# Optimization experiments

Hardware: AMD Instinct MI355X
Metric: run time of the kernel (lower is better)

Reference implementation:

```python
import jax, jax.numpy as jnp
import numpy as np

D_MODEL, D_HEAD, N_HEAD, PERIOD = 1024, 64, 16, 30
B, T1, T2 = 2, 2048, 2048


def setup_inputs() -> dict:
    key = jax.random.key(0)
    ks = jax.random.split(key, 7)
    s_in = 1.0 / np.sqrt(D_MODEL)
    s_out = 1.0 / np.sqrt(N_HEAD * D_HEAD)
    return {
        "x": jax.random.normal(ks[0], (B, T1, D_MODEL), dtype=jnp.float32),
        "context": jax.random.normal(ks[1], (B, T2, D_MODEL), dtype=jnp.float32),
        "Wq": jax.random.uniform(ks[2], (N_HEAD * D_HEAD, D_MODEL), jnp.float32, -s_in, s_in),
        "Wk": jax.random.uniform(ks[3], (N_HEAD * D_HEAD, D_MODEL), jnp.float32, -s_in, s_in),
        "Wv": jax.random.uniform(ks[4], (N_HEAD * D_HEAD, D_MODEL), jnp.float32, -s_in, s_in),
        "Wo": jax.random.uniform(ks[5], (D_MODEL, N_HEAD * D_HEAD), jnp.float32, -s_out, s_out),
        "bo": jax.random.uniform(ks[6], (D_MODEL,), jnp.float32, -s_out, s_out),
    }


def reference(x, context, Wq, Wk, Wv, Wo, bo):
    Bx, T1x, _ = x.shape
    T2x = context.shape[1]
    scale = 1.0 / np.sqrt(D_HEAD).astype(np.float32)
    # projections (torch Linear: y = x @ W^T)
    q = (x @ Wq.T).reshape(Bx, T1x, N_HEAD, D_HEAD)
    k = (context @ Wk.T).reshape(Bx, T2x, N_HEAD, D_HEAD)
    v = (context @ Wv.T).reshape(Bx, T2x, N_HEAD, D_HEAD)
    # attention scores [B, H, T1, T2]
    scores = jnp.einsum('bihd,bjhd->bhij', q, k) * scale
    # ALiBi-style periodic distance bias
    dist = jnp.abs(jnp.arange(T1x)[:, None] - jnp.arange(T2x)[None, :])  # [T1,T2]
    bias = -(dist // PERIOD).astype(jnp.float32)                          # [T1,T2]
    head_scale = jnp.power(2.0, -jnp.arange(1, N_HEAD + 1, dtype=jnp.float32))
    biased = scores + bias[None, None, :, :] * head_scale[None, :, None, None]
    attn = jax.nn.softmax(biased, axis=-1)
    out = jnp.einsum('bhij,bjhd->bihd', attn, v).reshape(Bx, T1x, N_HEAD * D_HEAD)
    # output projection; dropout is identity in eval mode
    return out @ Wo.T + bo
```

## Files before the change

### kernel.cpp

```cpp
#include <hip/hip_runtime.h>
#include <hip/hip_fp16.h>

typedef _Float16 f16;
typedef __attribute__((ext_vector_type(8))) _Float16 f16x8;
typedef __attribute__((ext_vector_type(4))) _Float16 f16x4;
typedef __attribute__((ext_vector_type(2))) __fp16 fp16x2;
typedef __attribute__((ext_vector_type(4))) float f32x4;
typedef __attribute__((ext_vector_type(16))) float f32x16;

#define DM 1024
#define NH 16
#define DH 64
#define TT 2048
#define LOG2E 1.4426950408889634f
#define QSCALE 0.18033688f

#define SB0 __builtin_amdgcn_sched_barrier(0)
#define LGKM0 asm volatile("s_waitcnt lgkmcnt(0)" ::: "memory")

__global__ __launch_bounds__(256) void cvt_all(const float* __restrict__ x, const float* __restrict__ cx,
                                               const float* __restrict__ wq, const float* __restrict__ wk,
                                               const float* __restrict__ wv, const float* __restrict__ wo,
                                               f16* __restrict__ xb, f16* __restrict__ cb,
                                               f16* __restrict__ wqb, f16* __restrict__ wkb,
                                               f16* __restrict__ wvb, f16* __restrict__ wob,
                                               f16* __restrict__ FBf) {
  int idx = blockIdx.x * 256 + threadIdx.x;
  int stride = gridDim.x * 256;
  for (int i = idx; i < 3670016; i += stride) {
    if (i >= 3145728) {
      int c = i - 3145728;
      int half = c & 1, lane = (c >> 1) & 63, kvt = (c >> 7) & 63, qt = c >> 13;
      int qi = qt * 32 + (lane & 31);
      int jb = kvt * 32 + 16 * half + 8 * (lane >> 5);
      f16x8 v;
#pragma unroll
      for (int e = 0; e < 8; e++) {
        int d = qi - (jb + e); d = (d < 0) ? -d : d;
        v[e] = (f16)(d / 30);
      }
      reinterpret_cast<f16x8*>(FBf)[c] = v;
      continue;
    }
    const float* src; f16* dst; int off; float s = 1.0f;
    if (i < 2097152) {
      if (i < 1048576) { src = x; dst = xb; off = i; }
      else { src = cx; dst = cb; off = i - 1048576; }
    } else {
      int j = i - 2097152;
      int wsel = j >> 18;
      off = j & 262143;
      if (wsel == 0) { src = wq; dst = wqb; s = QSCALE; }
      else if (wsel == 1) { src = wk; dst = wkb; }
      else if (wsel == 2) { src = wv; dst = wvb; }
      else { src = wo; dst = wob; }
    }
    float4 v = reinterpret_cast<const float4*>(src)[off];
    f16x4 o = { (f16)(v.x * s), (f16)(v.y * s), (f16)(v.z * s), (f16)(v.w * s) };
    reinterpret_cast<f16x4*>(dst)[off] = o;
  }
}

__device__ __forceinline__ void gemm_mainloop(const f16* __restrict__ A, const f16* __restrict__ W,
                                              int bm, int bn, f16 (*As)[4096], f16 (*Bs)[4096],
                                              f32x4 (&acc)[4][4]) {
  int t = threadIdx.x;
  int w = t >> 6;
  int lane = t & 63, lr = lane & 15, g = lane >> 4;
  int wr = w >> 1, wc = w & 1;
  int scol = ((t & 3) ^ ((t >> 3) & 3)) * 8;
  const f16* a0 = A + (size_t)(bm + (t >> 2)) * DM + scol;
  const f16* a1 = a0 + (size_t)64 * DM;
  const f16* b0 = W + (size_t)(bn + (t >> 2)) * DM + scol;
  const f16* b1 = b0 + (size_t)64 * DM;
  int szg = ((lr >> 1) & 3) << 4;

  f16x8 rA0, rA1, rB0, rB1;
  auto LOADR = [&](int kt) {
    rA0 = *reinterpret_cast<const f16x8*>(a0 + kt);
    rA1 = *reinterpret_cast<const f16x8*>(a1 + kt);
    rB0 = *reinterpret_cast<const f16x8*>(b0 + kt);
    rB1 = *reinterpret_cast<const f16x8*>(b1 + kt);
  };
  auto WRITE = [&](int bufi) {
    char* Ab = (char*)As[bufi];
    char* Bb = (char*)Bs[bufi];
    *reinterpret_cast<f16x8*>(Ab + t * 16) = rA0;
    *reinterpret_cast<f16x8*>(Ab + 4096 + t * 16) = rA1;
    *reinterpret_cast<f16x8*>(Bb + t * 16) = rB0;
    *reinterpret_cast<f16x8*>(Bb + 4096 + t * 16) = rB1;
  };
  auto CMPG = [&](int bufi) {
    const char* Ab = (const char*)As[bufi];
    const char* Bb = (const char*)Bs[bufi];
    f16x8 af[4], bf[4];
#pragma unroll
    for (int mi = 0; mi < 4; mi++) {
      int row = wr * 64 + mi * 16 + lr;
      af[mi] = *reinterpret_cast<const f16x8*>(Ab + row * 64 + ((g << 4) ^ szg));
    }
#pragma unroll
    for (int ni = 0; ni < 4; ni++) {
      int row = wc * 64 + ni * 16 + lr;
      bf[ni] = *reinterpret_cast<const f16x8*>(Bb + row * 64 + ((g << 4) ^ szg));
    }
    __builtin_amdgcn_s_setprio(1);
#pragma unroll
    for (int mi = 0; mi < 4; mi++)
#pragma unroll
      for (int ni = 0; ni < 4; ni++)
        acc[mi][ni] = __builtin_amdgcn_mfma_f32_16x16x32_f16(af[mi], bf[ni], acc[mi][ni], 0, 0, 0);
    __builtin_amdgcn_s_setprio(0);
  };

  LOADR(0);
  WRITE(0);
  LOADR(32);
  LGKM0;
  __builtin_amdgcn_s_barrier();
  SB0;

#pragma unroll 1
  for (int tp = 0; tp < 16; tp++) {
    int s0 = 2 * tp;
    CMPG(0);
    WRITE(1);
    if (s0 + 2 < 32) LOADR((s0 + 2) * 32);
    LGKM0;
    __builtin_amdgcn_s_barrier();
    SB0;
    CMPG(1);
    if (s0 + 2 < 32) {
      WRITE(0);
      if (s0 + 3 < 32) LOADR((s0 + 3) * 32);
      LGKM0;
      __builtin_amdgcn_s_barrier();
      SB0;
    }
  }
}

__global__ __launch_bounds__(256) void qkv_gemm(const f16* __restrict__ xb, const f16* __restrict__ cb,
                                                const f16* __restrict__ wq, const f16* __restrict__ wk,
                                                const f16* __restrict__ wv,
                                                f16* __restrict__ Qo, f16* __restrict__ Ko,
                                                f16* __restrict__ Vt) {
  __shared__ f16 As[2][4096];
  __shared__ f16 Bs[2][4096];
  int o = blockIdx.x;
  int lin = (o & 7) * 96 + (o >> 3);
  int gid = lin >> 8;
  int bid = lin & 255;
  int bm = (bid >> 3) * 128, bn = (bid & 7) * 128;
  const f16* A = (gid == 0) ? xb : cb;
  const f16* W = (gid == 0) ? wq : ((gid == 1) ? wk : wv);
  f32x4 acc[4][4] = {};
  gemm_mainloop(A, W, bm, bn, As, Bs, acc);

  int t = threadIdx.x, w = t >> 6, lane = t & 63, lr = lane & 15, g = lane >> 4;
  int wr = w >> 1, wc = w & 1;
  if (gid < 2) {
    f16* out = (gid == 0) ? Qo : Ko;
#pragma unroll
    for (int mi = 0; mi < 4; mi++) {
      int m0 = bm + wr * 64 + mi * 16 + 4 * g;
      int b = m0 >> 11, i0 = m0 & 2047;
#pragma unroll
      for (int ni = 0; ni < 4; ni++) {
        int n = bn + wc * 64 + ni * 16 + lr;
        int h = n >> 6, d = n & 63;
        size_t base = (((size_t)(b * NH + h)) * TT + i0) * DH + d;
#pragma unroll
        for (int r = 0; r < 4; r++)
          out[base + (size_t)r * DH] = (f16)acc[mi][ni][r];
      }
    }
  } else {
#pragma unroll
    for (int mi = 0; mi < 4; mi++) {
      int m0 = bm + wr * 64 + mi * 16 + 4 * g;
      int b = m0 >> 11, j0 = m0 & 2047;
#pragma unroll
      for (int ni = 0; ni < 4; ni++) {
        int n = bn + wc * 64 + ni * 16 + lr;
        int h = n >> 6, d = n & 63;
        f16x4 pk = { (f16)acc[mi][ni][0], (f16)acc[mi][ni][1],
                     (f16)acc[mi][ni][2], (f16)acc[mi][ni][3] };
        *reinterpret_cast<f16x4*>(&Vt[(((size_t)(b * NH + h)) * DH + d) * TT + j0]) = pk;
      }
    }
  }
}

__global__ __launch_bounds__(256) void out_gemm(const f16* __restrict__ Ob, const f16* __restrict__ wo,
                                                const float* __restrict__ bo, float* __restrict__ Y) {
  __shared__ f16 As[2][4096];
  __shared__ f16 Bs[2][4096];
  int o = blockIdx.x;
  int bid = (o & 7) * 32 + (o >> 3);
  int bm = (bid >> 3) * 128, bn = (bid & 7) * 128;
  f32x4 acc[4][4] = {};
  gemm_mainloop(Ob, wo, bm, bn, As, Bs, acc);
  int t = threadIdx.x, w = t >> 6, lane = t & 63, lr = lane & 15, g = lane >> 4;
  int wr = w >> 1, wc = w & 1;
#pragma unroll
  for (int mi = 0; mi < 4; mi++) {
    int m0 = bm + wr * 64 + mi * 16 + 4 * g;
#pragma unroll
    for (int ni = 0; ni < 4; ni++) {
      int n = bn + wc * 64 + ni * 16 + lr;
      float bias = bo[n];
#pragma unroll
      for (int r = 0; r < 4; r++)
        Y[(size_t)(m0 + r) * DM + n] = acc[mi][ni][r] + bias;
    }
  }
}

struct FB4 { f16x8 a, b, c, d; };

__global__ __launch_bounds__(256, 2) void attn_kernel(const f16* __restrict__ Q, const f16* __restrict__ K,
                                                      const f16* __restrict__ V, const f16* __restrict__ FBf,
                                                      f16* __restrict__ O) {
  __shared__ f16 KV[2][8192];
  int o = blockIdx.x;
  int xcd = o & 7, idx = o >> 3;
  int bh = 4 * xcd + (idx >> 4), qblk = idx & 15;
  int h = bh & 15, b = bh >> 4;
  int tt = threadIdx.x, w = tt >> 6, lane = tt & 63;
  int col = lane & 31, hi = lane >> 5;
  int qi = qblk * 128 + w * 32 + col;

  const f16* qp = Q + ((size_t)bh * TT + qi) * DH + hi * 8;
  f16x8 qf[4];
#pragma unroll
  for (int s = 0; s < 4; s++) qf[s] = *reinterpret_cast<const f16x8*>(qp + 16 * s);

  const float nc2 = -exp2f(-(float)(h + 1)) * LOG2E;
  int qtp = qblk * 4 + w;
  const f16x8* fbp = reinterpret_cast<const f16x8*>(FBf) + ((size_t)qtp << 13) + (lane << 1);

  f32x4 rsv = { 0.f, 0.f, 0.f, 0.f };
  f32x16 oacc0 = {}, oacc1 = {};

  int rho0 = tt >> 3, G = tt & 7;
  int f0 = (rho0 & 7) ^ (3 * ((rho0 >> 4) & 1));
  int J0 = (rho0 & 19) | ((rho0 & 4) << 1) | ((rho0 & 8) >> 1);
  const f16* kp0 = K + ((size_t)bh * TT + J0) * DH + (G ^ f0) * 8;
  const f16* kp1 = K + ((size_t)bh * TT + 32 + J0) * DH + (G ^ f0) * 8;
  const f16* vp0 = V + ((size_t)bh * DH + rho0) * TT + (G ^ f0) * 8;
  const f16* vp1 = V + ((size_t)bh * DH + 32 + rho0) * TT + (G ^ f0) * 8;

  f16x8 r0, r1, r2, r3;
  auto LOADR = [&](int kv0) {
    r0 = *reinterpret_cast<const f16x8*>(kp0 + (size_t)kv0 * DH);
    r1 = *reinterpret_cast<const f16x8*>(kp1 + (size_t)kv0 * DH);
    r2 = *reinterpret_cast<const f16x8*>(vp0 + kv0);
    r3 = *reinterpret_cast<const f16x8*>(vp1 + kv0);
  };
  auto WRITE = [&](int bufi) {
    char* base = (char*)KV[bufi];
    *reinterpret_cast<f16x8*>(base + tt * 16) = r0;
    *reinterpret_cast<f16x8*>(base + 4096 + tt * 16) = r1;
    *reinterpret_cast<f16x8*>(base + 8192 + tt * 16) = r2;
    *reinterpret_cast<f16x8*>(base + 12288 + tt * 16) = r3;
  };

  int fcol = (col & 7) ^ (3 * ((col >> 4) & 1));
  int kb0 = col * 128;
  int ksw[4];
#pragma unroll
  for (int s = 0; s < 4; s++) ksw[s] = ((2 * s + hi) ^ fcol) << 4;

  auto FBLOAD = [&](int t) {
    FB4 f;
    f.a = fbp[256 * t];
    f.b = fbp[256 * t + 1];
    f.c = fbp[256 * t + 128];
    f.d = fbp[256 * t + 129];
    return f;
  };

  auto CMP = [&](int bufi, const FB4& fb) {
    const char* Kb = (const char*)KV[bufi];
    f32x16 S0 = {}, S1 = {};
    __builtin_amdgcn_s_setprio(1);
#pragma unroll
    for (int s = 0; s < 4; s++) {
      f16x8 ka0 = *reinterpret_cast<const f16x8*>(Kb + kb0 + ksw[s]);
      f16x8 ka1 = *reinterpret_cast<const f16x8*>(Kb + 4096 + kb0 + ksw[s]);
      S0 = __builtin_amdgcn_mfma_f32_32x32x16_f16(ka0, qf[s], S0, 0, 0, 0);
      S1 = __builtin_amdgcn_mfma_f32_32x32x16_f16(ka1, qf[s], S1, 0, 0, 0);
    }
    __builtin_amdgcn_s_setprio(0);
    float p0[16], p1[16];
#pragma unroll
    for (int r = 0; r < 16; r++) {
      float fb0 = (float)((r < 8) ? fb.a[r] : fb.b[r - 8]);
      float fb1 = (float)((r < 8) ? fb.c[r] : fb.d[r - 8]);
      p0[r] = __builtin_amdgcn_exp2f(fmaf(fb0, nc2, S0[r]));
      p1[r] = __builtin_amdgcn_exp2f(fmaf(fb1, nc2, S1[r]));
    }
#pragma unroll
    for (int r = 0; r < 4; r++) {
      f32x4 pa = { p0[4 * r], p0[4 * r + 1], p0[4 * r + 2], p0[4 * r + 3] };
      f32x4 pc = { p1[4 * r], p1[4 * r + 1], p1[4 * r + 2], p1[4 * r + 3] };
      rsv += pa + pc;
    }
    f16x8 pb[4];
#pragma unroll
    for (int s2 = 0; s2 < 2; s2++) {
      union { f16x8 v; fp16x2 hh[4]; } u0, u1;
#pragma unroll
      for (int q2 = 0; q2 < 4; q2++) {
        u0.hh[q2] = __builtin_amdgcn_cvt_pkrtz(p0[8 * s2 + 2 * q2], p0[8 * s2 + 2 * q2 + 1]);
        u1.hh[q2] = __builtin_amdgcn_cvt_pkrtz(p1[8 * s2 + 2 * q2], p1[8 * s2 + 2 * q2 + 1]);
      }
      pb[s2] = u0.v; pb[2 + s2] = u1.v;
    }
    __builtin_amdgcn_s_setprio(1);
#pragma unroll
    for (int s2 = 0; s2 < 4; s2++) {
      f16x8 va0 = *reinterpret_cast<const f16x8*>(Kb + 8192 + kb0 + ksw[s2]);
      f16x8 va1 = *reinterpret_cast<const f16x8*>(Kb + 12288 + kb0 + ksw[s2]);
      oacc0 = __builtin_amdgcn_mfma_f32_32x32x16_f16(va0, pb[s2], oacc0, 0, 0, 0);
      oacc1 = __builtin_amdgcn_mfma_f32_32x32x16_f16(va1, pb[s2], oacc1, 0, 0, 0);
    }
    __builtin_amdgcn_s_setprio(0);
  };

  LOADR(0);
  WRITE(0);
  LOADR(64);
  FB4 fA = FBLOAD(0);
  FB4 fB = FBLOAD(1);
  LGKM0;
  __builtin_amdgcn_s_barrier();
  SB0;

#pragma unroll 1
  for (int tp = 0; tp < 16; tp++) {
    int t0 = 2 * tp;
    CMP(0, fA);
    WRITE(1);
    if (t0 + 2 < 32) { LOADR((t0 + 2) << 6); fA = FBLOAD(t0 + 2); }
    LGKM0;
    __builtin_amdgcn_s_barrier();
    SB0;
    CMP(1, fB);
    if (t0 + 2 < 32) {
      WRITE(0);
      if (t0 + 3 < 32) { LOADR((t0 + 3) << 6); fB = FBLOAD(t0 + 3); }
      LGKM0;
      __builtin_amdgcn_s_barrier();
      SB0;
    }
  }

  float lsum = (rsv[0] + rsv[1]) + (rsv[2] + rsv[3]);
  lsum += __shfl_xor(lsum, 32, 64);
  float inv = __builtin_amdgcn_rcpf(lsum);

  size_t ob = ((size_t)b * TT + qi) * DM + h * DH + 4 * hi;
  const f32x16* oa[2] = { &oacc0, &oacc1 };
#pragma unroll
  for (int db = 0; db < 2; db++)
#pragma unroll
    for (int a = 0; a < 4; a++) {
      f16x4 o4 = { (f16)((*oa[db])[4 * a] * inv),     (f16)((*oa[db])[4 * a + 1] * inv),
                   (f16)((*oa[db])[4 * a + 2] * inv), (f16)((*oa[db])[4 * a + 3] * inv) };
      *reinterpret_cast<f16x4*>(&O[ob + 32 * db + 8 * a]) = o4;
    }
}

extern "C" void kernel_launch(void* const* d_in, const int* in_sizes, int n_in,
                              void* d_out, int out_size, void* d_ws, size_t ws_size,
                              hipStream_t stream) {
  const float* x  = (const float*)d_in[0];
  const float* cx = (const float*)d_in[1];
  const float* Wq = (const float*)d_in[2];
  const float* Wk = (const float*)d_in[3];
  const float* Wv = (const float*)d_in[4];
  const float* Wo = (const float*)d_in[5];
  const float* bo = (const float*)d_in[6];
  float* Y = (float*)d_out;

  const size_t NTOK = (size_t)2 * TT;
  f16* p = (f16*)d_ws;
  f16* xb  = p; p += NTOK * DM;
  f16* cb  = p; p += NTOK * DM;
  f16* wqb = p; p += (size_t)DM * DM;
  f16* wkb = p; p += (size_t)DM * DM;
  f16* wvb = p; p += (size_t)DM * DM;
  f16* wob = p; p += (size_t)DM * DM;
  f16* Qb  = p; p += NTOK * DM;
  f16* Kb  = p; p += NTOK * DM;
  f16* Vtb = p; p += NTOK * DM;
  f16* Ob  = p; p += NTOK * DM;
  f16* FBt = p;

  cvt_all<<<2048, 256, 0, stream>>>(x, cx, Wq, Wk, Wv, Wo, xb, cb, wqb, wkb, wvb, wob, FBt);
  qkv_gemm<<<768, 256, 0, stream>>>(xb, cb, wqb, wkb, wvb, Qb, Kb, Vtb);
  attn_kernel<<<512, 256, 0, stream>>>(Qb, Kb, Vtb, FBt, Ob);
  out_gemm<<<256, 256, 0, stream>>>(Ob, wob, bo, Y);
}
```

Before: 124.6 us.

## Split attention KV range in two and merge partial results in output GEMM

The attention grid doubles so each block handles half of the key/value sequence. Each block writes an unnormalized f16 partial output plus its row sum, and the occupancy hint rises from 2 to 4 blocks per CU. The output-projection GEMM now loads both partial outputs, adds them, and normalizes by the summed row sums while staging A tiles into shared memory, which removes the separate normalization pass. The aim is more parallelism and better latency hiding in attention. In exchange the output GEMM reads more global memory, and the tighter launch bound may cause register spills.

```diff
diff --git a/kernel.cpp b/kernel.cpp
--- a/kernel.cpp
+++ b/kernel.cpp
@@ -192,17 +192,110 @@
   }
 }
 
-__global__ __launch_bounds__(256) void out_gemm(const f16* __restrict__ Ob, const f16* __restrict__ wo,
+__global__ __launch_bounds__(256) void out_gemm(const f16* __restrict__ O0, const f16* __restrict__ O1,
+                                                const float* __restrict__ Ls,
+                                                const f16* __restrict__ wo,
                                                 const float* __restrict__ bo, float* __restrict__ Y) {
   __shared__ f16 As[2][4096];
   __shared__ f16 Bs[2][4096];
   int o = blockIdx.x;
   int bid = (o & 7) * 32 + (o >> 3);
   int bm = (bid >> 3) * 128, bn = (bid & 7) * 128;
-  f32x4 acc[4][4] = {};
-  gemm_mainloop(Ob, wo, bm, bn, As, Bs, acc);
   int t = threadIdx.x, w = t >> 6, lane = t & 63, lr = lane & 15, g = lane >> 4;
   int wr = w >> 1, wc = w & 1;
+  int scol = ((t & 3) ^ ((t >> 3) & 3)) * 8;
+  int row = bm + (t >> 2);
+  const f16* a00 = O0 + (size_t)row * DM + scol;
+  const f16* a01 = O1 + (size_t)row * DM + scol;
+  const f16* b0 = wo + (size_t)(bn + (t >> 2)) * DM + scol;
+  const f16* b1 = b0 + (size_t)64 * DM;
+  int bb = row >> 11, ii = row & 2047;
+  const float* ls0 = Ls + (size_t)(bb * NH) * TT + ii;
+  const float* ls1 = ls0 + 65536;
+  int szg = ((lr >> 1) & 3) << 4;
+
+  f32x4 acc[4][4] = {};
+  f16x8 rA0a, rA0b, rA1a, rA1b, rB0, rB1;
+  float l0a, l1a, l0b, l1b;
+
+  auto LOADR = [&](int kt) {
+    rA0a = *reinterpret_cast<const f16x8*>(a00 + kt);
+    rA0b = *reinterpret_cast<const f16x8*>(a01 + kt);
+    rA1a = *reinterpret_cast<const f16x8*>(a00 + (size_t)64 * DM + kt);
+    rA1b = *reinterpret_cast<const f16x8*>(a01 + (size_t)64 * DM + kt);
+    rB0 = *reinterpret_cast<const f16x8*>(b0 + kt);
+    rB1 = *reinterpret_cast<const f16x8*>(b1 + kt);
+    int h = (kt + scol) >> 6;
+    l0a = ls0[h * TT];
+    l1a = ls1[h * TT];
+    l0b = ls0[h * TT + 64];
+    l1b = ls1[h * TT + 64];
+  };
+  auto WRITE = [&](int bufi) {
+    float inva = __builtin_amdgcn_rcpf(l0a + l1a);
+    float invb = __builtin_amdgcn_rcpf(l0b + l1b);
+    f16x8 uA0, uA1;
+#pragma unroll
+    for (int e = 0; e < 8; e++) {
+      uA0[e] = (f16)(((float)rA0a[e] + (float)rA0b[e]) * inva);
+      uA1[e] = (f16)(((float)rA1a[e] + (float)rA1b[e]) * invb);
+    }
+    char* Ab = (char*)As[bufi];
+    char* Bb = (char*)Bs[bufi];
+    *reinterpret_cast<f16x8*>(Ab + t * 16) = uA0;
+    *reinterpret_cast<f16x8*>(Ab + 4096 + t * 16) = uA1;
+    *reinterpret_cast<f16x8*>(Bb + t * 16) = rB0;
+    *reinterpret_cast<f16x8*>(Bb + 4096 + t * 16) = rB1;
+  };
+  auto CMPG = [&](int bufi) {
+    const char* Ab = (const char*)As[bufi];
+    const char* Bb = (const char*)Bs[bufi];
+    f16x8 af[4], bf[4];
+#pragma unroll
+    for (int mi = 0; mi < 4; mi++) {
+      int rw = wr * 64 + mi * 16 + lr;
+      af[mi] = *reinterpret_cast<const f16x8*>(Ab + rw * 64 + ((g << 4) ^ szg));
+    }
+#pragma unroll
+    for (int ni = 0; ni < 4; ni++) {
+      int rw = wc * 64 + ni * 16 + lr;
+      bf[ni] = *reinterpret_cast<const f16x8*>(Bb + rw * 64 + ((g << 4) ^ szg));
+    }
+    __builtin_amdgcn_s_setprio(1);
+#pragma unroll
+    for (int mi = 0; mi < 4; mi++)
+#pragma unroll
+      for (int ni = 0; ni < 4; ni++)
+        acc[mi][ni] = __builtin_amdgcn_mfma_f32_16x16x32_f16(af[mi], bf[ni], acc[mi][ni], 0, 0, 0);
+    __builtin_amdgcn_s_setprio(0);
+  };
+
+  LOADR(0);
+  WRITE(0);
+  LOADR(32);
+  LGKM0;
+  __builtin_amdgcn_s_barrier();
+  SB0;
+
+#pragma unroll 1
+  for (int tp = 0; tp < 16; tp++) {
+    int s0 = 2 * tp;
+    CMPG(0);
+    WRITE(1);
+    if (s0 + 2 < 32) LOADR((s0 + 2) * 32);
+    LGKM0;
+    __builtin_amdgcn_s_barrier();
+    SB0;
+    CMPG(1);
+    if (s0 + 2 < 32) {
+      WRITE(0);
+      if (s0 + 3 < 32) LOADR((s0 + 3) * 32);
+      LGKM0;
+      __builtin_amdgcn_s_barrier();
+      SB0;
+    }
+  }
+
 #pragma unroll
   for (int mi = 0; mi < 4; mi++) {
     int m0 = bm + wr * 64 + mi * 16 + 4 * g;
@@ -219,17 +312,21 @@
 
 struct FB4 { f16x8 a, b, c, d; };
 
-__global__ __launch_bounds__(256, 2) void attn_kernel(const f16* __restrict__ Q, const f16* __restrict__ K,
+__global__ __launch_bounds__(256, 4) void attn_kernel(const f16* __restrict__ Q, const f16* __restrict__ K,
                                                       const f16* __restrict__ V, const f16* __restrict__ FBf,
-                                                      f16* __restrict__ O) {
+                                                      f16* __restrict__ O0, f16* __restrict__ O1,
+                                                      float* __restrict__ Ls) {
   __shared__ f16 KV[2][8192];
   int o = blockIdx.x;
   int xcd = o & 7, idx = o >> 3;
-  int bh = 4 * xcd + (idx >> 4), qblk = idx & 15;
+  int bh = 4 * xcd + (idx >> 5);
+  int rem = idx & 31;
+  int qblk = rem >> 1, half = rem & 1;
   int h = bh & 15, b = bh >> 4;
   int tt = threadIdx.x, w = tt >> 6, lane = tt & 63;
   int col = lane & 31, hi = lane >> 5;
   int qi = qblk * 128 + w * 32 + col;
+  int kvbase = half << 10;
 
   const f16* qp = Q + ((size_t)bh * TT + qi) * DH + hi * 8;
   f16x8 qf[4];
@@ -239,6 +336,7 @@
   const float nc2 = -exp2f(-(float)(h + 1)) * LOG2E;
   int qtp = qblk * 4 + w;
   const f16x8* fbp = reinterpret_cast<const f16x8*>(FBf) + ((size_t)qtp << 13) + (lane << 1);
+  int tb = half * 16;
 
   f32x4 rsv = { 0.f, 0.f, 0.f, 0.f };
   f32x16 oacc0 = {}, oacc1 = {};
@@ -246,10 +344,10 @@
   int rho0 = tt >> 3, G = tt & 7;
   int f0 = (rho0 & 7) ^ (3 * ((rho0 >> 4) & 1));
   int J0 = (rho0 & 19) | ((rho0 & 4) << 1) | ((rho0 & 8) >> 1);
-  const f16* kp0 = K + ((size_t)bh * TT + J0) * DH + (G ^ f0) * 8;
-  const f16* kp1 = K + ((size_t)bh * TT + 32 + J0) * DH + (G ^ f0) * 8;
-  const f16* vp0 = V + ((size_t)bh * DH + rho0) * TT + (G ^ f0) * 8;
-  const f16* vp1 = V + ((size_t)bh * DH + 32 + rho0) * TT + (G ^ f0) * 8;
+  const f16* kp0 = K + ((size_t)bh * TT + kvbase + J0) * DH + (G ^ f0) * 8;
+  const f16* kp1 = K + ((size_t)bh * TT + kvbase + 32 + J0) * DH + (G ^ f0) * 8;
+  const f16* vp0 = V + ((size_t)bh * DH + rho0) * TT + kvbase + (G ^ f0) * 8;
+  const f16* vp1 = V + ((size_t)bh * DH + 32 + rho0) * TT + kvbase + (G ^ f0) * 8;
 
   f16x8 r0, r1, r2, r3;
   auto LOADR = [&](int kv0) {
@@ -332,25 +430,25 @@
   LOADR(0);
   WRITE(0);
   LOADR(64);
-  FB4 fA = FBLOAD(0);
-  FB4 fB = FBLOAD(1);
+  FB4 fA = FBLOAD(tb);
+  FB4 fB = FBLOAD(tb + 1);
   LGKM0;
   __builtin_amdgcn_s_barrier();
   SB0;
 
 #pragma unroll 1
-  for (int tp = 0; tp < 16; tp++) {
+  for (int tp = 0; tp < 8; tp++) {
     int t0 = 2 * tp;
     CMP(0, fA);
     WRITE(1);
-    if (t0 + 2 < 32) { LOADR((t0 + 2) << 6); fA = FBLOAD(t0 + 2); }
+    if (t0 + 2 < 16) { LOADR((t0 + 2) << 6); fA = FBLOAD(tb + t0 + 2); }
     LGKM0;
     __builtin_amdgcn_s_barrier();
     SB0;
     CMP(1, fB);
-    if (t0 + 2 < 32) {
+    if (t0 + 2 < 16) {
       WRITE(0);
-      if (t0 + 3 < 32) { LOADR((t0 + 3) << 6); fB = FBLOAD(t0 + 3); }
+      if (t0 + 3 < 16) { LOADR((t0 + 3) << 6); fB = FBLOAD(tb + t0 + 3); }
       LGKM0;
       __builtin_amdgcn_s_barrier();
       SB0;
@@ -359,18 +457,19 @@
 
   float lsum = (rsv[0] + rsv[1]) + (rsv[2] + rsv[3]);
   lsum += __shfl_xor(lsum, 32, 64);
-  float inv = __builtin_amdgcn_rcpf(lsum);
-
+
+  f16* Op = half ? O1 : O0;
   size_t ob = ((size_t)b * TT + qi) * DM + h * DH + 4 * hi;
   const f32x16* oa[2] = { &oacc0, &oacc1 };
 #pragma unroll
   for (int db = 0; db < 2; db++)
 #pragma unroll
     for (int a = 0; a < 4; a++) {
-      f16x4 o4 = { (f16)((*oa[db])[4 * a] * inv),     (f16)((*oa[db])[4 * a + 1] * inv),
-                   (f16)((*oa[db])[4 * a + 2] * inv), (f16)((*oa[db])[4 * a + 3] * inv) };
-      *reinterpret_cast<f16x4*>(&O[ob + 32 * db + 8 * a]) = o4;
-    }
+      f16x4 o4 = { (f16)(*oa[db])[4 * a], (f16)(*oa[db])[4 * a + 1],
+                   (f16)(*oa[db])[4 * a + 2], (f16)(*oa[db])[4 * a + 3] };
+      *reinterpret_cast<f16x4*>(&Op[ob + 32 * db + 8 * a]) = o4;
+    }
+  if (lane < 32) Ls[half * 65536 + bh * TT + qi] = lsum;
 }
 
 extern "C" void kernel_launch(void* const* d_in, const int* in_sizes, int n_in,
@@ -397,10 +496,12 @@
   f16* Kb  = p; p += NTOK * DM;
   f16* Vtb = p; p += NTOK * DM;
   f16* Ob  = p; p += NTOK * DM;
-  f16* FBt = p;
+  f16* FBt = p; p += (size_t)8 * 1024 * 1024 / 2;
+  float* Ls = (float*)p;
+  f16* Ob1 = xb;
 
   cvt_all<<<2048, 256, 0, stream>>>(x, cx, Wq, Wk, Wv, Wo, xb, cb, wqb, wkb, wvb, wob, FBt);
   qkv_gemm<<<768, 256, 0, stream>>>(xb, cb, wqb, wkb, wvb, Qb, Kb, Vtb);
-  attn_kernel<<<512, 256, 0, stream>>>(Qb, Kb, Vtb, FBt, Ob);
-  out_gemm<<<256, 256, 0, stream>>>(Ob, wob, bo, Y);
+  attn_kernel<<<1024, 256, 0, stream>>>(Qb, Kb, Vtb, FBt, Ob, Ob1, Ls);
+  out_gemm<<<256, 256, 0, stream>>>(Ob, Ob1, Ls, wob, bo, Y);
 }
```

After: 331.6 us. 2.66x slower.
